# Optimization experiments

Hardware: AMD Instinct MI355X
Metric: run time of the kernel (lower is better)

The kernel has to match this reference:

```python
import jax, jax.numpy as jnp
import numpy as np
from jax import lax

K = 3          # spline order
G = 5          # grid intervals
R0, R1 = -4.0, 4.0  # grid_range
IN, HID, OUT = 32, 128, 16
BATCH, SEQ = 256, 512


def make_grid(n_in):
    # extended knot vector: G+2K+1 knots per input, uniform spacing h
    h = (R1 - R0) / G
    knots = R0 + h * jnp.arange(-K, G + K + 1, dtype=jnp.float32)  # [G+2K+1]
    return jnp.broadcast_to(knots, (n_in, G + 2 * K + 1))


def b_splines(x, grid):
    # Cox-de Boor recursion. x: [B, n], grid: [n, G+2K+1] -> basis [B, n, G+K]
    xg = x[..., None]
    B = ((xg >= grid[:, :-1]) & (xg < grid[:, 1:])).astype(x.dtype)
    for d in range(1, K + 1):
        B = ((xg - grid[:, :-(d + 1)]) / (grid[:, d:-1] - grid[:, :-(d + 1)]) * B[..., :-1]
             + (grid[:, d + 1:] - xg) / (grid[:, d + 1:] - grid[:, 1:-d]) * B[..., 1:])
    return B


def kan_layer(x, coef, scale_base, scale_sp, grid):
    # y[b,o] = sum_i scale_base[i,o]*silu(x[b,i]) + scale_sp[i,o]*spline_io(x[b,i])
    base = jax.nn.silu(x)                               # [B, n_in]
    Bsp = b_splines(x, grid)                            # [B, n_in, G+K]
    spline = jnp.einsum('bik,iok->bio', Bsp, coef)      # [B, n_in, n_out]
    return (jnp.einsum('bi,io->bo', base, scale_base)
            + jnp.einsum('bio,io->bo', spline, scale_sp))


def setup_inputs() -> dict:
    key = jax.random.key(0)
    ks = jax.random.split(key, 7)
    x = jax.random.normal(ks[0], (BATCH, SEQ, IN), dtype=jnp.float32)
    coef1 = jax.random.normal(ks[1], (IN + HID, HID, G + K), dtype=jnp.float32) * 0.1
    sb1 = jax.random.normal(ks[2], (IN + HID, HID), dtype=jnp.float32) * 0.05
    sp1 = jax.random.normal(ks[3], (IN + HID, HID), dtype=jnp.float32) * 0.05
    coef2 = jax.random.normal(ks[4], (HID, OUT, G + K), dtype=jnp.float32) * 0.1
    sb2 = jax.random.normal(ks[5], (HID, OUT), dtype=jnp.float32) * 0.05
    sp2 = jax.random.normal(ks[6], (HID, OUT), dtype=jnp.float32) * 0.05
    return {"x": x, "coef1": coef1, "sb1": sb1, "sp1": sp1,
            "coef2": coef2, "sb2": sb2, "sp2": sp2}


def reference(x, coef1, sb1, sp1, coef2, sb2, sp2):
    grid1 = make_grid(IN + HID)
    grid2 = make_grid(HID)

    def step(h, x_t):
        combined = jnp.concatenate([x_t, h], axis=1)        # [B, IN+HID]
        h_new = kan_layer(combined, coef1, sb1, sp1, grid1)  # [B, HID]
        out_t = kan_layer(h_new, coef2, sb2, sp2, grid2)     # [B, OUT]
        return h_new, out_t

    h0 = jnp.zeros((x.shape[0], HID), dtype=x.dtype)
    _, outs = lax.scan(step, h0, jnp.swapaxes(x, 0, 1))  # outs: [T, B, OUT]
    # original stacks all timestep outputs then returns outputs[:, -1, :]
    return outs[-1]
```

## Files before the change

kernel.cpp:

```cpp
#include <hip/hip_runtime.h>
#include <hip/hip_bf16.h>

#define NIN 32
#define NHID 128
#define NOUT 16
#define SEQT 512
#define NB 256
#define RPW 40

typedef __attribute__((ext_vector_type(8))) short s16x8;
typedef __attribute__((ext_vector_type(4))) float f32x4;

__device__ __forceinline__ unsigned int f2bfbits(float f) {
    unsigned int u = __float_as_uint(f);
    return (u + 0x7fffu + ((u >> 16) & 1u)) >> 16;
}
__device__ __forceinline__ unsigned int packbf(float lo, float hi) {
    return f2bfbits(lo) | (f2bfbits(hi) << 16);
}

__device__ __forceinline__ float fsilu(float c) {
    return c * __builtin_amdgcn_rcpf(1.f + __expf(-c));
}

struct E8 { float e0, e1, e2, e3, e4, e5, e6, e7, sil; };

__device__ __forceinline__ E8 feat8(float c) {
    const float t0 = -8.8f, inv_h = 0.625f;
    float u  = (c - t0) * inv_h;
    float uf = floorf(u);
    int   m0 = (int)uf;
    bool valid = (m0 >= 0) && (m0 <= 10);
    float f   = u - uf;
    float omf = 1.0f - f;
    float f2 = f * f, f3 = f2 * f;
    float omf3 = omf * omf * omf;
    const float c6 = 0.16666667f;
    float v0 = omf3 * c6;
    float v1 = __builtin_fmaf(3.0f, f3, __builtin_fmaf(-6.0f, f2, 4.0f)) * c6;
    float v2 = __builtin_fmaf(-3.0f, f3, __builtin_fmaf(3.0f, f + f2, 1.0f)) * c6;
    float v3 = f3 * c6;
    int jb = m0 - 3;
    int js = jb < 0 ? 0 : (jb > 4 ? 4 : jb);
    E8 r;
    r.sil = fsilu(c);
#define SELK(k) { int d = (k) - js; int idx = (k) - jb; \
    float s = (idx == 0) ? v0 : (idx == 1) ? v1 : (idx == 2) ? v2 : (idx == 3) ? v3 : 0.f; \
    r.e##k = (valid && d >= 0 && d <= 3) ? s : 0.f; }
    SELK(0) SELK(1) SELK(2) SELK(3) SELK(4) SELK(5) SELK(6) SELK(7)
#undef SELK
    return r;
}

__device__ __forceinline__ float sb1_pad(const float* __restrict__ sb1, int wbase, int r, int oo) {
    int rr = (r < RPW) ? r : 0;
    float v = sb1[(wbase + rr) * NHID + oo];
    return (r < RPW) ? v : 0.f;
}

#define O4(X) X(0) X(1) X(2) X(3)
#define K10(X) X(0) X(1) X(2) X(3) X(4) X(5) X(6) X(7) X(8) X(9)

__attribute__((amdgpu_waves_per_eu(2, 2)))
__global__ void __launch_bounds__(512)
kan_seq(const float* __restrict__ x,
        const float* __restrict__ coef1,
        const float* __restrict__ sb1,
        const float* __restrict__ sp1,
        const float* __restrict__ coef2,
        const float* __restrict__ sb2,
        const float* __restrict__ sp2,
        float* __restrict__ out)
{
    __shared__ __align__(16) unsigned int scr[8][RPW][4];
    __shared__ __align__(16) unsigned short scrS[8][64];
    __shared__ __align__(16) float part[2][4][NHID];
    __shared__ float Hf[NHID][9];

    const int tid  = threadIdx.x;
    const int b    = blockIdx.x;
    const int lane = tid & 63;
    const int w    = tid >> 6;
    const int kq   = w >> 1;
    const int oh   = w & 1;
    const int arow = lane & 15;
    const int agrp = lane >> 4;
    const int recL = kq * RPW + lane;

#define DECLW(k) uint4 wf##k##_0, wf##k##_1, wf##k##_2, wf##k##_3;
    K10(DECLW) DECLW(10) DECLW(11)
#undef DECLW

#define INITW1(k,t) { \
    int rec = kq * RPW + (k) * 4 + agrp; \
    int oo  = oh * 64 + (t) * 16 + arow; \
    const float4* cp = (const float4*)(coef1 + (size_t)(rec * NHID + oo) * 8); \
    float sp = sp1[rec * NHID + oo]; \
    float4 c0 = cp[0], c1 = cp[1]; \
    wf##k##_##t = make_uint4(packbf(sp * c0.x, sp * c0.y), packbf(sp * c0.z, sp * c0.w), \
                             packbf(sp * c1.x, sp * c1.y), packbf(sp * c1.z, sp * c1.w)); }
#define INITWK(k) INITW1(k,0) INITW1(k,1) INITW1(k,2) INITW1(k,3)
    K10(INITWK)
#undef INITWK
#undef INITW1

#define INITS1(k,t) { \
    int oo = oh * 64 + (t) * 16 + arow; \
    int rbs = ((k) - 10) * 32 + agrp * 8; \
    int wbase = kq * RPW; \
    float e0 = sb1_pad(sb1, wbase, rbs + 0, oo), e1 = sb1_pad(sb1, wbase, rbs + 1, oo); \
    float e2 = sb1_pad(sb1, wbase, rbs + 2, oo), e3 = sb1_pad(sb1, wbase, rbs + 3, oo); \
    float e4 = sb1_pad(sb1, wbase, rbs + 4, oo), e5 = sb1_pad(sb1, wbase, rbs + 5, oo); \
    float e6 = sb1_pad(sb1, wbase, rbs + 6, oo), e7 = sb1_pad(sb1, wbase, rbs + 7, oo); \
    wf##k##_##t = make_uint4(packbf(e0, e1), packbf(e2, e3), packbf(e4, e5), packbf(e6, e7)); }
#define INITSK(k) INITS1(k,0) INITS1(k,1) INITS1(k,2) INITS1(k,3)
    INITSK(10) INITSK(11)
#undef INITSK
#undef INITS1

    ((float*)part)[tid] = 0.f;
    ((float*)part)[tid + 512] = 0.f;
    if (tid < 256) ((unsigned int*)scrS)[tid] = 0u;
    float xv = 0.f;
    if (w < 2 && lane < NIN) xv = x[(size_t)b * SEQT * NIN + lane];
    const f32x4 zq = {0.f, 0.f, 0.f, 0.f};
    __syncthreads();

    for (int t = 0; t < SEQT; ++t) {
        const int rb = t & 1, wb = rb ^ 1;

        float xv_use = xv;
        if (w < 2 && lane < NIN) {
            int tn = (t + 1 < SEQT) ? (t + 1) : t;
            xv = x[((size_t)b * SEQT + tn) * NIN + lane];
        }
        if (lane < RPW) {
            float c;
            if (recL < NIN) c = xv_use;
            else {
                int hi = recL - NIN;
                c = (part[rb][0][hi] + part[rb][1][hi])
                  + (part[rb][2][hi] + part[rb][3][hi]);
            }
            E8 ft = feat8(c);
            uint4 pk;
            pk.x = packbf(ft.e0, ft.e1); pk.y = packbf(ft.e2, ft.e3);
            pk.z = packbf(ft.e4, ft.e5); pk.w = packbf(ft.e6, ft.e7);
            *(uint4*)&scr[w][lane][0] = pk;
            scrS[w][lane] = (unsigned short)f2bfbits(ft.sil);
        }

        asm volatile("s_waitcnt lgkmcnt(0)" ::: "memory");
        __builtin_amdgcn_sched_barrier(0);
        uint4 bq0 = *(const uint4*)&scr[w][agrp][0];
        uint4 bq1 = *(const uint4*)&scr[w][4 + agrp][0];

        f32x4 ac0, ac1, ac2, ac3;
#define MMROW0(k, bqv) { s16x8 bb_ = __builtin_bit_cast(s16x8, bqv); \
        ac0 = __builtin_amdgcn_mfma_f32_16x16x32_bf16(__builtin_bit_cast(s16x8, wf##k##_0), bb_, zq, 0, 0, 0); \
        ac1 = __builtin_amdgcn_mfma_f32_16x16x32_bf16(__builtin_bit_cast(s16x8, wf##k##_1), bb_, zq, 0, 0, 0); \
        ac2 = __builtin_amdgcn_mfma_f32_16x16x32_bf16(__builtin_bit_cast(s16x8, wf##k##_2), bb_, zq, 0, 0, 0); \
        ac3 = __builtin_amdgcn_mfma_f32_16x16x32_bf16(__builtin_bit_cast(s16x8, wf##k##_3), bb_, zq, 0, 0, 0); }
#define MMROW(k, bqv) { s16x8 bb_ = __builtin_bit_cast(s16x8, bqv); \
        ac0 = __builtin_amdgcn_mfma_f32_16x16x32_bf16(__builtin_bit_cast(s16x8, wf##k##_0), bb_, ac0, 0, 0, 0); \
        ac1 = __builtin_amdgcn_mfma_f32_16x16x32_bf16(__builtin_bit_cast(s16x8, wf##k##_1), bb_, ac1, 0, 0, 0); \
        ac2 = __builtin_amdgcn_mfma_f32_16x16x32_bf16(__builtin_bit_cast(s16x8, wf##k##_2), bb_, ac2, 0, 0, 0); \
        ac3 = __builtin_amdgcn_mfma_f32_16x16x32_bf16(__builtin_bit_cast(s16x8, wf##k##_3), bb_, ac3, 0, 0, 0); }
        MMROW0(0, bq0)  uint4 bq2 = *(const uint4*)&scr[w][8 + agrp][0];
        MMROW(1, bq1)   uint4 bq3 = *(const uint4*)&scr[w][12 + agrp][0];
        MMROW(2, bq2)   uint4 bq4 = *(const uint4*)&scr[w][16 + agrp][0];
        MMROW(3, bq3)   uint4 bq5 = *(const uint4*)&scr[w][20 + agrp][0];
        MMROW(4, bq4)   uint4 bq6 = *(const uint4*)&scr[w][24 + agrp][0];
        MMROW(5, bq5)   uint4 bq7 = *(const uint4*)&scr[w][28 + agrp][0];
        MMROW(6, bq6)   uint4 bq8 = *(const uint4*)&scr[w][32 + agrp][0];
        MMROW(7, bq7)   uint4 bq9 = *(const uint4*)&scr[w][36 + agrp][0];
        MMROW(8, bq8)   uint4 bs0 = *(const uint4*)&scrS[w][agrp * 8];
        MMROW(9, bq9)   uint4 bs1 = *(const uint4*)&scrS[w][32 + agrp * 8];
        MMROW(10, bs0)
        MMROW(11, bs1)
#undef MMROW
#undef MMROW0

#define WRR(tt) if (arow == (tt)) \
            *(f32x4*)&part[wb][kq][oh * 64 + (tt) * 16 + (agrp << 2)] = ac##tt;
        O4(WRR)
#undef WRR
        __syncthreads();
    }

    if (tid < NHID) {
        float c = (part[0][0][tid] + part[0][1][tid])
                + (part[0][2][tid] + part[0][3][tid]);
        E8 ft = feat8(c);
        Hf[tid][0] = ft.e0; Hf[tid][1] = ft.e1; Hf[tid][2] = ft.e2; Hf[tid][3] = ft.e3;
        Hf[tid][4] = ft.e4; Hf[tid][5] = ft.e5; Hf[tid][6] = ft.e6; Hf[tid][7] = ft.e7;
        Hf[tid][8] = ft.sil;
    }
    __syncthreads();
    if (tid < 128) {
        int o2 = tid & 15, isg = tid >> 4;
        float acc = 0.f;
        for (int q = 0; q < 16; ++q) {
            int i = isg * 16 + q;
            const float* c2 = coef2 + (size_t)(i * NOUT + o2) * 8;
            float s = 0.f;
            #pragma unroll
            for (int k = 0; k < 8; ++k) s += Hf[i][k] * c2[k];
            acc += Hf[i][8] * sb2[i * NOUT + o2] + sp2[i * NOUT + o2] * s;
        }
        ((float*)part)[isg * 16 + o2] = acc;
    }
    __syncthreads();
    if (tid < NOUT) {
        float a = 0.f;
        #pragma unroll
        for (int g = 0; g < 8; ++g) a += ((float*)part)[g * 16 + tid];
        out[(size_t)b * NOUT + tid] = a;
    }
}

extern "C" void kernel_launch(void* const* d_in, const int* in_sizes, int n_in,
                              void* d_out, int out_size, void* d_ws, size_t ws_size,
                              hipStream_t stream) {
    kan_seq<<<NB, 512, 0, stream>>>(
        (const float*)d_in[0], (const float*)d_in[1], (const float*)d_in[2],
        (const float*)d_in[3], (const float*)d_in[4], (const float*)d_in[5],
        (const float*)d_in[6], (float*)d_out);
}
```

Before: 1.219 ms.

## Repartition layer-1 work into 2 K-halves by 4 output quarters per wave

New measurement: 1.218 ms. About the same (-0.1%).

```diff
diff --git a/kernel.cpp b/kernel.cpp
--- a/kernel.cpp
+++ b/kernel.cpp
@@ -6,7 +6,7 @@
 #define NOUT 16
 #define SEQT 512
 #define NB 256
-#define RPW 40
+#define RPH 80
 
 typedef __attribute__((ext_vector_type(8))) short s16x8;
 typedef __attribute__((ext_vector_type(4))) float f32x4;
@@ -52,14 +52,14 @@
     return r;
 }
 
-__device__ __forceinline__ float sb1_pad(const float* __restrict__ sb1, int wbase, int r, int oo) {
-    int rr = (r < RPW) ? r : 0;
-    float v = sb1[(wbase + rr) * NHID + oo];
-    return (r < RPW) ? v : 0.f;
-}
-
-#define O4(X) X(0) X(1) X(2) X(3)
-#define K10(X) X(0) X(1) X(2) X(3) X(4) X(5) X(6) X(7) X(8) X(9)
+__device__ __forceinline__ float sb1_pad(const float* __restrict__ sb1, int base, int r, int oo) {
+    int rr = (r < RPH) ? r : 0;
+    float v = sb1[(base + rr) * NHID + oo];
+    return (r < RPH) ? v : 0.f;
+}
+
+#define K20(X) X(0) X(1) X(2) X(3) X(4) X(5) X(6) X(7) X(8) X(9) \
+               X(10) X(11) X(12) X(13) X(14) X(15) X(16) X(17) X(18) X(19)
 
 __attribute__((amdgpu_waves_per_eu(2, 2)))
 __global__ void __launch_bounds__(512)
@@ -72,57 +72,55 @@
         const float* __restrict__ sp2,
         float* __restrict__ out)
 {
-    __shared__ __align__(16) unsigned int scr[8][RPW][4];
-    __shared__ __align__(16) unsigned short scrS[8][64];
-    __shared__ __align__(16) float part[2][4][NHID];
+    __shared__ __align__(16) unsigned int scr[2][RPH][4];
+    __shared__ __align__(16) unsigned short scrS[2][96];
+    __shared__ __align__(16) float part[2][2][NHID];
     __shared__ float Hf[NHID][9];
 
     const int tid  = threadIdx.x;
     const int b    = blockIdx.x;
     const int lane = tid & 63;
     const int w    = tid >> 6;
-    const int kq   = w >> 1;
-    const int oh   = w & 1;
+    const int kh   = w >> 2;
+    const int oq   = w & 3;
     const int arow = lane & 15;
     const int agrp = lane >> 4;
-    const int recL = kq * RPW + lane;
-
-#define DECLW(k) uint4 wf##k##_0, wf##k##_1, wf##k##_2, wf##k##_3;
-    K10(DECLW) DECLW(10) DECLW(11)
+    const int rec20 = oq * 20 + lane;
+
+#define DECLW(k) uint4 wf##k##_0, wf##k##_1;
+    K20(DECLW) DECLW(20) DECLW(21) DECLW(22)
 #undef DECLW
 
 #define INITW1(k,t) { \
-    int rec = kq * RPW + (k) * 4 + agrp; \
-    int oo  = oh * 64 + (t) * 16 + arow; \
+    int rec = kh * RPH + (k) * 4 + agrp; \
+    int oo  = oq * 32 + (t) * 16 + arow; \
     const float4* cp = (const float4*)(coef1 + (size_t)(rec * NHID + oo) * 8); \
     float sp = sp1[rec * NHID + oo]; \
     float4 c0 = cp[0], c1 = cp[1]; \
     wf##k##_##t = make_uint4(packbf(sp * c0.x, sp * c0.y), packbf(sp * c0.z, sp * c0.w), \
                              packbf(sp * c1.x, sp * c1.y), packbf(sp * c1.z, sp * c1.w)); }
-#define INITWK(k) INITW1(k,0) INITW1(k,1) INITW1(k,2) INITW1(k,3)
-    K10(INITWK)
+#define INITWK(k) INITW1(k,0) INITW1(k,1)
+    K20(INITWK)
 #undef INITWK
+
+#define INITS1(k,t) { \
+    int oo = oq * 32 + (t) * 16 + arow; \
+    int rbs = ((k) - 20) * 32 + agrp * 8; \
+    int base = kh * RPH; \
+    float e0 = sb1_pad(sb1, base, rbs + 0, oo), e1 = sb1_pad(sb1, base, rbs + 1, oo); \
+    float e2 = sb1_pad(sb1, base, rbs + 2, oo), e3 = sb1_pad(sb1, base, rbs + 3, oo); \
+    float e4 = sb1_pad(sb1, base, rbs + 4, oo), e5 = sb1_pad(sb1, base, rbs + 5, oo); \
+    float e6 = sb1_pad(sb1, base, rbs + 6, oo), e7 = sb1_pad(sb1, base, rbs + 7, oo); \
+    wf##k##_##t = make_uint4(packbf(e0, e1), packbf(e2, e3), packbf(e4, e5), packbf(e6, e7)); }
+    INITS1(20,0) INITS1(20,1) INITS1(21,0) INITS1(21,1) INITS1(22,0) INITS1(22,1)
+#undef INITS1
 #undef INITW1
 
-#define INITS1(k,t) { \
-    int oo = oh * 64 + (t) * 16 + arow; \
-    int rbs = ((k) - 10) * 32 + agrp * 8; \
-    int wbase = kq * RPW; \
-    float e0 = sb1_pad(sb1, wbase, rbs + 0, oo), e1 = sb1_pad(sb1, wbase, rbs + 1, oo); \
-    float e2 = sb1_pad(sb1, wbase, rbs + 2, oo), e3 = sb1_pad(sb1, wbase, rbs + 3, oo); \
-    float e4 = sb1_pad(sb1, wbase, rbs + 4, oo), e5 = sb1_pad(sb1, wbase, rbs + 5, oo); \
-    float e6 = sb1_pad(sb1, wbase, rbs + 6, oo), e7 = sb1_pad(sb1, wbase, rbs + 7, oo); \
-    wf##k##_##t = make_uint4(packbf(e0, e1), packbf(e2, e3), packbf(e4, e5), packbf(e6, e7)); }
-#define INITSK(k) INITS1(k,0) INITS1(k,1) INITS1(k,2) INITS1(k,3)
-    INITSK(10) INITSK(11)
-#undef INITSK
-#undef INITS1
-
     ((float*)part)[tid] = 0.f;
-    ((float*)part)[tid + 512] = 0.f;
-    if (tid < 256) ((unsigned int*)scrS)[tid] = 0u;
+    if (tid < 96) ((unsigned int*)scrS)[tid] = 0u;
+    const bool ldx = (kh == 0) && (lane < 20) && (rec20 < NIN);
     float xv = 0.f;
-    if (w < 2 && lane < NIN) xv = x[(size_t)b * SEQT * NIN + lane];
+    if (ldx) xv = x[(size_t)b * SEQT * NIN + rec20];
     const f32x4 zq = {0.f, 0.f, 0.f, 0.f};
     __syncthreads();
 
@@ -130,67 +128,71 @@
         const int rb = t & 1, wb = rb ^ 1;
 
         float xv_use = xv;
-        if (w < 2 && lane < NIN) {
+        if (ldx) {
             int tn = (t + 1 < SEQT) ? (t + 1) : t;
-            xv = x[((size_t)b * SEQT + tn) * NIN + lane];
+            xv = x[((size_t)b * SEQT + tn) * NIN + rec20];
         }
-        if (lane < RPW) {
+        if (lane < 20) {
+            int grec = kh * RPH + rec20;
             float c;
-            if (recL < NIN) c = xv_use;
+            if (grec < NIN) c = xv_use;
             else {
-                int hi = recL - NIN;
-                c = (part[rb][0][hi] + part[rb][1][hi])
-                  + (part[rb][2][hi] + part[rb][3][hi]);
+                int hi = grec - NIN;
+                c = part[rb][0][hi] + part[rb][1][hi];
             }
             E8 ft = feat8(c);
             uint4 pk;
             pk.x = packbf(ft.e0, ft.e1); pk.y = packbf(ft.e2, ft.e3);
             pk.z = packbf(ft.e4, ft.e5); pk.w = packbf(ft.e6, ft.e7);
-            *(uint4*)&scr[w][lane][0] = pk;
-            scrS[w][lane] = (unsigned short)f2bfbits(ft.sil);
+            *(uint4*)&scr[kh][rec20][0] = pk;
+            scrS[kh][rec20] = (unsigned short)f2bfbits(ft.sil);
         }
-
-        asm volatile("s_waitcnt lgkmcnt(0)" ::: "memory");
-        __builtin_amdgcn_sched_barrier(0);
-        uint4 bq0 = *(const uint4*)&scr[w][agrp][0];
-        uint4 bq1 = *(const uint4*)&scr[w][4 + agrp][0];
-
-        f32x4 ac0, ac1, ac2, ac3;
+        __syncthreads();
+
+        f32x4 ac0, ac1;
 #define MMROW0(k, bqv) { s16x8 bb_ = __builtin_bit_cast(s16x8, bqv); \
         ac0 = __builtin_amdgcn_mfma_f32_16x16x32_bf16(__builtin_bit_cast(s16x8, wf##k##_0), bb_, zq, 0, 0, 0); \
-        ac1 = __builtin_amdgcn_mfma_f32_16x16x32_bf16(__builtin_bit_cast(s16x8, wf##k##_1), bb_, zq, 0, 0, 0); \
-        ac2 = __builtin_amdgcn_mfma_f32_16x16x32_bf16(__builtin_bit_cast(s16x8, wf##k##_2), bb_, zq, 0, 0, 0); \
-        ac3 = __builtin_amdgcn_mfma_f32_16x16x32_bf16(__builtin_bit_cast(s16x8, wf##k##_3), bb_, zq, 0, 0, 0); }
+        ac1 = __builtin_amdgcn_mfma_f32_16x16x32_bf16(__builtin_bit_cast(s16x8, wf##k##_1), bb_, zq, 0, 0, 0); }
 #define MMROW(k, bqv) { s16x8 bb_ = __builtin_bit_cast(s16x8, bqv); \
         ac0 = __builtin_amdgcn_mfma_f32_16x16x32_bf16(__builtin_bit_cast(s16x8, wf##k##_0), bb_, ac0, 0, 0, 0); \
-        ac1 = __builtin_amdgcn_mfma_f32_16x16x32_bf16(__builtin_bit_cast(s16x8, wf##k##_1), bb_, ac1, 0, 0, 0); \
-        ac2 = __builtin_amdgcn_mfma_f32_16x16x32_bf16(__builtin_bit_cast(s16x8, wf##k##_2), bb_, ac2, 0, 0, 0); \
-        ac3 = __builtin_amdgcn_mfma_f32_16x16x32_bf16(__builtin_bit_cast(s16x8, wf##k##_3), bb_, ac3, 0, 0, 0); }
-        MMROW0(0, bq0)  uint4 bq2 = *(const uint4*)&scr[w][8 + agrp][0];
-        MMROW(1, bq1)   uint4 bq3 = *(const uint4*)&scr[w][12 + agrp][0];
-        MMROW(2, bq2)   uint4 bq4 = *(const uint4*)&scr[w][16 + agrp][0];
-        MMROW(3, bq3)   uint4 bq5 = *(const uint4*)&scr[w][20 + agrp][0];
-        MMROW(4, bq4)   uint4 bq6 = *(const uint4*)&scr[w][24 + agrp][0];
-        MMROW(5, bq5)   uint4 bq7 = *(const uint4*)&scr[w][28 + agrp][0];
-        MMROW(6, bq6)   uint4 bq8 = *(const uint4*)&scr[w][32 + agrp][0];
-        MMROW(7, bq7)   uint4 bq9 = *(const uint4*)&scr[w][36 + agrp][0];
-        MMROW(8, bq8)   uint4 bs0 = *(const uint4*)&scrS[w][agrp * 8];
-        MMROW(9, bq9)   uint4 bs1 = *(const uint4*)&scrS[w][32 + agrp * 8];
-        MMROW(10, bs0)
-        MMROW(11, bs1)
+        ac1 = __builtin_amdgcn_mfma_f32_16x16x32_bf16(__builtin_bit_cast(s16x8, wf##k##_1), bb_, ac1, 0, 0, 0); }
+        uint4 bqa = *(const uint4*)&scr[kh][agrp][0];
+        uint4 bqb = *(const uint4*)&scr[kh][4 + agrp][0];
+        MMROW0(0, bqa)  bqa = *(const uint4*)&scr[kh][8 + agrp][0];
+        MMROW(1, bqb)   bqb = *(const uint4*)&scr[kh][12 + agrp][0];
+        MMROW(2, bqa)   bqa = *(const uint4*)&scr[kh][16 + agrp][0];
+        MMROW(3, bqb)   bqb = *(const uint4*)&scr[kh][20 + agrp][0];
+        MMROW(4, bqa)   bqa = *(const uint4*)&scr[kh][24 + agrp][0];
+        MMROW(5, bqb)   bqb = *(const uint4*)&scr[kh][28 + agrp][0];
+        MMROW(6, bqa)   bqa = *(const uint4*)&scr[kh][32 + agrp][0];
+        MMROW(7, bqb)   bqb = *(const uint4*)&scr[kh][36 + agrp][0];
+        MMROW(8, bqa)   bqa = *(const uint4*)&scr[kh][40 + agrp][0];
+        MMROW(9, bqb)   bqb = *(const uint4*)&scr[kh][44 + agrp][0];
+        MMROW(10, bqa)  bqa = *(const uint4*)&scr[kh][48 + agrp][0];
+        MMROW(11, bqb)  bqb = *(const uint4*)&scr[kh][52 + agrp][0];
+        MMROW(12, bqa)  bqa = *(const uint4*)&scr[kh][56 + agrp][0];
+        MMROW(13, bqb)  bqb = *(const uint4*)&scr[kh][60 + agrp][0];
+        MMROW(14, bqa)  bqa = *(const uint4*)&scr[kh][64 + agrp][0];
+        MMROW(15, bqb)  bqb = *(const uint4*)&scr[kh][68 + agrp][0];
+        MMROW(16, bqa)  bqa = *(const uint4*)&scr[kh][72 + agrp][0];
+        MMROW(17, bqb)  bqb = *(const uint4*)&scr[kh][76 + agrp][0];
+        MMROW(18, bqa)  bqa = *(const uint4*)&scrS[kh][agrp * 8];
+        MMROW(19, bqb)  bqb = *(const uint4*)&scrS[kh][32 + agrp * 8];
+        MMROW(20, bqa)  bqa = *(const uint4*)&scrS[kh][64 + agrp * 8];
+        MMROW(21, bqb)
+        MMROW(22, bqa)
 #undef MMROW
 #undef MMROW0
 
-#define WRR(tt) if (arow == (tt)) \
-            *(f32x4*)&part[wb][kq][oh * 64 + (tt) * 16 + (agrp << 2)] = ac##tt;
-        O4(WRR)
-#undef WRR
+        if (arow == 0)
+            *(f32x4*)&part[wb][kh][oq * 32 + (agrp << 2)] = ac0;
+        if (arow == 1)
+            *(f32x4*)&part[wb][kh][oq * 32 + 16 + (agrp << 2)] = ac1;
         __syncthreads();
     }
 
     if (tid < NHID) {
-        float c = (part[0][0][tid] + part[0][1][tid])
-                + (part[0][2][tid] + part[0][3][tid]);
+        float c = part[0][0][tid] + part[0][1][tid];
         E8 ft = feat8(c);
         Hf[tid][0] = ft.e0; Hf[tid][1] = ft.e1; Hf[tid][2] = ft.e2; Hf[tid][3] = ft.e3;
         Hf[tid][4] = ft.e4; Hf[tid][5] = ft.e5; Hf[tid][6] = ft.e6; Hf[tid][7] = ft.e7;
@@ -208,13 +210,13 @@
             for (int k = 0; k < 8; ++k) s += Hf[i][k] * c2[k];
             acc += Hf[i][8] * sb2[i * NOUT + o2] + sp2[i * NOUT + o2] * s;
         }
-        ((float*)part)[isg * 16 + o2] = acc;
+        ((float*)scr)[isg * 16 + o2] = acc;
     }
     __syncthreads();
     if (tid < NOUT) {
         float a = 0.f;
         #pragma unroll
-        for (int g = 0; g < 8; ++g) a += ((float*)part)[g * 16 + tid];
+        for (int g = 0; g < 8; ++g) a += ((float*)scr)[g * 16 + tid];
         out[(size_t)b * NOUT + tid] = a;
     }
 }
```
